# Optimization experiments

Measured on AMD Instinct MI355X. Metric: run time of the kernel, lower is better.

Reference implementation:

```python
import jax, jax.numpy as jnp
import numpy as np

EMB, KDIM, B, S = 1024, 64, 8, 2048

def setup_inputs() -> dict:
    key = jax.random.key(0)
    kx, kq, kk, kv1, kv2 = jax.random.split(key, 5)
    def xavier(k, shape):
        fan_in, fan_out = shape
        lim = (6.0 / (fan_in + fan_out)) ** 0.5
        return jax.random.uniform(k, shape, jnp.float32, -lim, lim)
    return {
        "x": jax.random.normal(kx, (B, S, EMB), jnp.float32),
        "w_q": xavier(kq, (EMB, KDIM)),
        "w_k": xavier(kk, (EMB, KDIM)),
        "w_v1": xavier(kv1, (EMB, KDIM)),
        "w_v2": xavier(kv2, (KDIM, EMB)),
    }

def reference(x, w_q, w_k, w_v1, w_v2) -> jnp.ndarray:
    # x: [B, S, E]
    seq = x.shape[1]
    queries = jnp.einsum("bse,ek->bsk", x, w_q)
    keys = jnp.einsum("bse,ek->bsk", x, w_k)
    scale = w_q.shape[1] ** -0.5
    scores = jnp.einsum("bqk,bsk->bqs", queries, keys) * scale  # [B, S, S]
    causal = jnp.tril(jnp.ones((seq, seq), dtype=bool))  # True = keep
    scores = jnp.where(causal[None, :, :], scores, -jnp.inf)
    attn = jax.nn.softmax(scores, axis=-1)
    values = jnp.einsum("bsk,ke->bse", jnp.einsum("bse,ek->bsk", x, w_v1), w_v2)
    return jnp.einsum("bqs,bse->bqe", attn, values)
```

## Files before the change

### kernel.cpp

```cpp
#include <hip/hip_runtime.h>

typedef _Float16 f16_t;
typedef __attribute__((ext_vector_type(8))) _Float16 f16x8;
typedef __attribute__((ext_vector_type(4))) _Float16 f16x4;
typedef __attribute__((ext_vector_type(4))) float f32x4;

#define MFMA16(a, b, c) __builtin_amdgcn_mfma_f32_16x16x32_f16((a), (b), (c), 0, 0, 0)


extern "C" __global__ __launch_bounds__(256) void prep_k(
    const float* __restrict__ wq, const float* __restrict__ wk,
    const float* __restrict__ wv1, const float* __restrict__ wv2,
    f16_t* __restrict__ WT, f16_t* __restrict__ WV2T) {
  int idx = blockIdx.x * 256 + threadIdx.x;
  if (idx < 196608) {
    int j = idx >> 16;
    int r = idx & 65535;
    int n = r >> 10;
    int e = r & 1023;
    const float* w = (j == 0) ? wq : ((j == 1) ? wk : wv1);
    float v = w[e * 64 + n];
    if (j == 0) v *= 0.125f;
    WT[idx] = (f16_t)v;
  } else if (idx < 262144) {
    int r = idx - 196608;
    int e = r >> 6, k = r & 63;
    WV2T[r] = (f16_t)wv2[k * 1024 + e];
  }
}

extern "C" __global__ __launch_bounds__(256) void proj_k(
    const float* __restrict__ x, const f16_t* __restrict__ WT,
    f16_t* __restrict__ Qg, f16_t* __restrict__ Kg, f16_t* __restrict__ Vtg) {
  __shared__ __align__(16) f16_t xs[64][72];
  __shared__ __align__(16) f16_t wsh[192][72];
  const int t = threadIdx.x;
  const int wave = t >> 6, lane = t & 63;
  const int quad = lane >> 4, ln = lane & 15;
  const int r0 = blockIdx.x * 64;

  f32x4 acc[4][3];
#pragma unroll
  for (int mt = 0; mt < 4; ++mt)
#pragma unroll
    for (int nn = 0; nn < 3; ++nn) acc[mt][nn] = (f32x4){0.f, 0.f, 0.f, 0.f};

  float4 xreg[4];
  f16x8 wreg[6];
#pragma unroll
  for (int i = 0; i < 4; ++i) {
    int flat = t + i * 256;
    int row = flat >> 4, c4 = (flat & 15) * 4;
    xreg[i] = *(const float4*)&x[(size_t)(r0 + row) * 1024 + c4];
  }
#pragma unroll
  for (int i = 0; i < 6; ++i) {
    int flat = t + i * 256;
    int row = flat >> 3, c8 = (flat & 7) * 8;
    wreg[i] = *(const f16x8*)&WT[row * 1024 + c8];
  }

  for (int ec = 0; ec < 16; ++ec) {
    __syncthreads();
#pragma unroll
    for (int i = 0; i < 4; ++i) {
      int flat = t + i * 256;
      int row = flat >> 4, c4 = (flat & 15) * 4;
      f16x4 h;
      h[0] = (f16_t)xreg[i].x; h[1] = (f16_t)xreg[i].y;
      h[2] = (f16_t)xreg[i].z; h[3] = (f16_t)xreg[i].w;
      *(f16x4*)&xs[row][c4] = h;
    }
#pragma unroll
    for (int i = 0; i < 6; ++i) {
      int flat = t + i * 256;
      int row = flat >> 3, c8 = (flat & 7) * 8;
      *(f16x8*)&wsh[row][c8] = wreg[i];
    }
    __syncthreads();
    if (ec < 15) {
      int e0 = (ec + 1) * 64;
#pragma unroll
      for (int i = 0; i < 4; ++i) {
        int flat = t + i * 256;
        int row = flat >> 4, c4 = (flat & 15) * 4;
        xreg[i] = *(const float4*)&x[(size_t)(r0 + row) * 1024 + e0 + c4];
      }
#pragma unroll
      for (int i = 0; i < 6; ++i) {
        int flat = t + i * 256;
        int row = flat >> 3, c8 = (flat & 7) * 8;
        wreg[i] = *(const f16x8*)&WT[row * 1024 + e0 + c8];
      }
    }
    f16x8 a0[4], a1[4];
#pragma unroll
    for (int mt = 0; mt < 4; ++mt) {
      a0[mt] = *(const f16x8*)&xs[mt * 16 + ln][quad * 8];
      a1[mt] = *(const f16x8*)&xs[mt * 16 + ln][32 + quad * 8];
    }
#pragma unroll
    for (int nn = 0; nn < 3; ++nn) {
      int nb = (wave * 3 + nn) * 16;
      f16x8 b0 = *(const f16x8*)&wsh[nb + ln][quad * 8];
      f16x8 b1 = *(const f16x8*)&wsh[nb + ln][32 + quad * 8];
#pragma unroll
      for (int mt = 0; mt < 4; ++mt) {
        acc[mt][nn] = MFMA16(a0[mt], b0, acc[mt][nn]);
        acc[mt][nn] = MFMA16(a1[mt], b1, acc[mt][nn]);
      }
    }
  }

  __syncthreads();
  f16_t* vt = &xs[0][0];
#pragma unroll
  for (int nn = 0; nn < 3; ++nn) {
    int col = (wave * 3 + nn) * 16 + ln;
    int j = col >> 6, cc = col & 63;
#pragma unroll
    for (int mt = 0; mt < 4; ++mt)
#pragma unroll
      for (int r = 0; r < 4; ++r) {
        int row = mt * 16 + quad * 4 + r;
        f16_t hv = (f16_t)acc[mt][nn][r];
        if (j == 0)      Qg[(size_t)(r0 + row) * 64 + cc] = hv;
        else if (j == 1) Kg[(size_t)(r0 + row) * 64 + cc] = hv;
        else             vt[cc * 72 + row] = hv;
      }
  }
  __syncthreads();
  {
    int bb = r0 >> 11, sblk = r0 & 2047;
#pragma unroll
    for (int i = 0; i < 2; ++i) {
      int flat = t + i * 256;
      int vrow = flat >> 3, c8 = (flat & 7) * 8;
      *(f16x8*)&Vtg[((size_t)bb * 64 + vrow) * 2048 + sblk + c8] =
          *(const f16x8*)&vt[vrow * 72 + c8];
    }
  }
}

extern "C" __global__ __launch_bounds__(256) void flash_k(
    const f16_t* __restrict__ Qg, const f16_t* __restrict__ Kg,
    const f16_t* __restrict__ Vtg, f16_t* __restrict__ O1) {
  __shared__ __align__(16) f16_t Ks[64][72];
  __shared__ __align__(16) f16_t Vs[64][72];
  __shared__ __align__(16) f16_t Ps[4][16][72];
  const int t = threadIdx.x;
  const int wave = t >> 6, lane = t & 63;
  const int quad = lane >> 4, ln = lane & 15;
  const int b = blockIdx.x >> 5, qt = blockIdx.x & 31;
  const int q0 = qt * 64;
  const size_t rbase = (size_t)b * 2048;

  f16x8 qa0, qa1;
  {
    size_t row = rbase + q0 + wave * 16 + ln;
    qa0 = *(const f16x8*)&Qg[row * 64 + quad * 8];
    qa1 = *(const f16x8*)&Qg[row * 64 + 32 + quad * 8];
  }
  float m[4], lsum[4];
  f32x4 oacc[4];
#pragma unroll
  for (int r = 0; r < 4; ++r) { m[r] = -__builtin_inff(); lsum[r] = 0.f; }
#pragma unroll
  for (int nt = 0; nt < 4; ++nt) oacc[nt] = (f32x4){0.f, 0.f, 0.f, 0.f};

  f16x8 kreg[2], vreg[2];
#pragma unroll
  for (int i = 0; i < 2; ++i) {
    int flat = t + i * 256;
    int row = flat >> 3, c8 = (flat & 7) * 8;
    kreg[i] = *(const f16x8*)&Kg[(rbase + row) * 64 + c8];
    vreg[i] = *(const f16x8*)&Vtg[((size_t)b * 64 + row) * 2048 + c8];
  }

  for (int st = 0; st <= qt; ++st) {
    __syncthreads();
#pragma unroll
    for (int i = 0; i < 2; ++i) {
      int flat = t + i * 256;
      int row = flat >> 3, c8 = (flat & 7) * 8;
      *(f16x8*)&Ks[row][c8] = kreg[i];
      *(f16x8*)&Vs[row][c8] = vreg[i];
    }
    __syncthreads();
    if (st < qt) {
      int s0n = (st + 1) * 64;
#pragma unroll
      for (int i = 0; i < 2; ++i) {
        int flat = t + i * 256;
        int row = flat >> 3, c8 = (flat & 7) * 8;
        kreg[i] = *(const f16x8*)&Kg[(rbase + s0n + row) * 64 + c8];
        vreg[i] = *(const f16x8*)&Vtg[((size_t)b * 64 + row) * 2048 + s0n + c8];
      }
    }
    f32x4 sc[4];
#pragma unroll
    for (int nt = 0; nt < 4; ++nt) {
      f16x8 b0 = *(const f16x8*)&Ks[nt * 16 + ln][quad * 8];
      f16x8 b1 = *(const f16x8*)&Ks[nt * 16 + ln][32 + quad * 8];
      f32x4 c = (f32x4){0.f, 0.f, 0.f, 0.f};
      c = MFMA16(qa0, b0, c);
      c = MFMA16(qa1, b1, c);
      sc[nt] = c;
    }
    if (st == qt) {
#pragma unroll
      for (int nt = 0; nt < 4; ++nt)
#pragma unroll
        for (int r = 0; r < 4; ++r)
          if (nt * 16 + ln > wave * 16 + quad * 4 + r) sc[nt][r] = -__builtin_inff();
    }
    float alpha[4], mn[4];
#pragma unroll
    for (int r = 0; r < 4; ++r) {
      float mx = fmaxf(fmaxf(sc[0][r], sc[1][r]), fmaxf(sc[2][r], sc[3][r]));
      mx = fmaxf(mx, __shfl_xor(mx, 1, 64));
      mx = fmaxf(mx, __shfl_xor(mx, 2, 64));
      mx = fmaxf(mx, __shfl_xor(mx, 4, 64));
      mx = fmaxf(mx, __shfl_xor(mx, 8, 64));
      mn[r] = fmaxf(m[r], mx);
      alpha[r] = __expf(m[r] - mn[r]);
      m[r] = mn[r];
    }
    float p[4][4];
#pragma unroll
    for (int nt = 0; nt < 4; ++nt)
#pragma unroll
      for (int r = 0; r < 4; ++r) p[nt][r] = __expf(sc[nt][r] - mn[r]);
#pragma unroll
    for (int r = 0; r < 4; ++r) {
      float s = (p[0][r] + p[1][r]) + (p[2][r] + p[3][r]);
      s += __shfl_xor(s, 1, 64);
      s += __shfl_xor(s, 2, 64);
      s += __shfl_xor(s, 4, 64);
      s += __shfl_xor(s, 8, 64);
      lsum[r] = lsum[r] * alpha[r] + s;
    }
#pragma unroll
    for (int nt = 0; nt < 4; ++nt)
#pragma unroll
      for (int r = 0; r < 4; ++r) oacc[nt][r] *= alpha[r];
#pragma unroll
    for (int nt = 0; nt < 4; ++nt)
#pragma unroll
      for (int r = 0; r < 4; ++r)
        Ps[wave][quad * 4 + r][nt * 16 + ln] = (f16_t)p[nt][r];
    f16x8 pa0 = *(const f16x8*)&Ps[wave][ln][quad * 8];
    f16x8 pa1 = *(const f16x8*)&Ps[wave][ln][32 + quad * 8];
#pragma unroll
    for (int nt = 0; nt < 4; ++nt) {
      f16x8 v0 = *(const f16x8*)&Vs[nt * 16 + ln][quad * 8];
      f16x8 v1 = *(const f16x8*)&Vs[nt * 16 + ln][32 + quad * 8];
      oacc[nt] = MFMA16(pa0, v0, oacc[nt]);
      oacc[nt] = MFMA16(pa1, v1, oacc[nt]);
    }
  }
  float inv[4];
#pragma unroll
  for (int r = 0; r < 4; ++r) inv[r] = 1.0f / lsum[r];
#pragma unroll
  for (int nt = 0; nt < 4; ++nt)
#pragma unroll
    for (int r = 0; r < 4; ++r) {
      size_t row = rbase + q0 + wave * 16 + quad * 4 + r;
      O1[row * 64 + nt * 16 + ln] = (f16_t)(oacc[nt][r] * inv[r]);
    }
}

extern "C" __global__ __launch_bounds__(256) void fproj_k(
    const f16_t* __restrict__ O1, const f16_t* __restrict__ WV2T,
    float* __restrict__ out) {
  const int t = threadIdx.x;
  const int wave = t >> 6, lane = t & 63;
  const int quad = lane >> 4, ln = lane & 15;
  const int r0 = blockIdx.x * 64;
  f16x8 a0[4], a1[4];
#pragma unroll
  for (int mt = 0; mt < 4; ++mt) {
    size_t row = (size_t)(r0 + mt * 16 + ln);
    a0[mt] = *(const f16x8*)&O1[row * 64 + quad * 8];
    a1[mt] = *(const f16x8*)&O1[row * 64 + 32 + quad * 8];
  }
#pragma unroll 4
  for (int nt = 0; nt < 16; ++nt) {
    int eb = wave * 256 + nt * 16;
    f16x8 b0 = *(const f16x8*)&WV2T[(eb + ln) * 64 + quad * 8];
    f16x8 b1 = *(const f16x8*)&WV2T[(eb + ln) * 64 + 32 + quad * 8];
#pragma unroll
    for (int mt = 0; mt < 4; ++mt) {
      f32x4 c = (f32x4){0.f, 0.f, 0.f, 0.f};
      c = MFMA16(a0[mt], b0, c);
      c = MFMA16(a1[mt], b1, c);
#pragma unroll
      for (int r = 0; r < 4; ++r)
        out[(size_t)(r0 + mt * 16 + quad * 4 + r) * 1024 + eb + ln] = c[r];
    }
  }
}

extern "C" void kernel_launch(void* const* d_in, const int* in_sizes, int n_in,
                              void* d_out, int out_size, void* d_ws, size_t ws_size,
                              hipStream_t stream) {
  const float* x   = (const float*)d_in[0];
  const float* wq  = (const float*)d_in[1];
  const float* wk  = (const float*)d_in[2];
  const float* wv1 = (const float*)d_in[3];
  const float* wv2 = (const float*)d_in[4];
  float* out = (float*)d_out;

  f16_t* WT   = (f16_t*)d_ws;
  f16_t* WV2T = WT + 196608;
  f16_t* Qg   = WV2T + 65536;
  f16_t* Kg   = Qg + 1048576;
  f16_t* Vtg  = Kg + 1048576;
  f16_t* O1   = Vtg + 1048576;

  prep_k <<<1024, 256, 0, stream>>>(wq, wk, wv1, wv2, WT, WV2T);
  proj_k <<<256, 256, 0, stream>>>(x, WT, Qg, Kg, Vtg);
  flash_k<<<256, 256, 0, stream>>>(Qg, Kg, Vtg, O1);
  fproj_k<<<256, 256, 0, stream>>>(O1, WV2T, out);
}
```

Before: 180.3 us.

## Split attention KV range across blocks with merge pass; halve projection tiles

The flash kernel now splits each query tile's causal key range into chunks of 8 key tiles, handled by separate blocks. Each block writes unnormalized partial outputs plus its row max and sum, and a new merge kernel combines them with log-sum-exp weighting. Projection and final-projection kernels use 32-row tiles, which doubles their grid size. The aim is to fix the low occupancy and causal load imbalance of 256 blocks on a large GPU, at the cost of partial-buffer traffic, an extra launch, and fp16 rounding of the unnormalized partials.

```diff
diff --git a/kernel.cpp b/kernel.cpp
--- a/kernel.cpp
+++ b/kernel.cpp
@@ -32,23 +32,23 @@
 extern "C" __global__ __launch_bounds__(256) void proj_k(
     const float* __restrict__ x, const f16_t* __restrict__ WT,
     f16_t* __restrict__ Qg, f16_t* __restrict__ Kg, f16_t* __restrict__ Vtg) {
-  __shared__ __align__(16) f16_t xs[64][72];
+  __shared__ __align__(16) f16_t xs[32][72];
   __shared__ __align__(16) f16_t wsh[192][72];
   const int t = threadIdx.x;
   const int wave = t >> 6, lane = t & 63;
   const int quad = lane >> 4, ln = lane & 15;
-  const int r0 = blockIdx.x * 64;
-
-  f32x4 acc[4][3];
-#pragma unroll
-  for (int mt = 0; mt < 4; ++mt)
+  const int r0 = blockIdx.x * 32;
+
+  f32x4 acc[2][3];
+#pragma unroll
+  for (int mt = 0; mt < 2; ++mt)
 #pragma unroll
     for (int nn = 0; nn < 3; ++nn) acc[mt][nn] = (f32x4){0.f, 0.f, 0.f, 0.f};
 
-  float4 xreg[4];
+  float4 xreg[2];
   f16x8 wreg[6];
 #pragma unroll
-  for (int i = 0; i < 4; ++i) {
+  for (int i = 0; i < 2; ++i) {
     int flat = t + i * 256;
     int row = flat >> 4, c4 = (flat & 15) * 4;
     xreg[i] = *(const float4*)&x[(size_t)(r0 + row) * 1024 + c4];
@@ -63,7 +63,7 @@
   for (int ec = 0; ec < 16; ++ec) {
     __syncthreads();
 #pragma unroll
-    for (int i = 0; i < 4; ++i) {
+    for (int i = 0; i < 2; ++i) {
       int flat = t + i * 256;
       int row = flat >> 4, c4 = (flat & 15) * 4;
       f16x4 h;
@@ -81,7 +81,7 @@
     if (ec < 15) {
       int e0 = (ec + 1) * 64;
 #pragma unroll
-      for (int i = 0; i < 4; ++i) {
+      for (int i = 0; i < 2; ++i) {
         int flat = t + i * 256;
         int row = flat >> 4, c4 = (flat & 15) * 4;
         xreg[i] = *(const float4*)&x[(size_t)(r0 + row) * 1024 + e0 + c4];
@@ -93,9 +93,9 @@
         wreg[i] = *(const f16x8*)&WT[row * 1024 + e0 + c8];
       }
     }
-    f16x8 a0[4], a1[4];
-#pragma unroll
-    for (int mt = 0; mt < 4; ++mt) {
+    f16x8 a0[2], a1[2];
+#pragma unroll
+    for (int mt = 0; mt < 2; ++mt) {
       a0[mt] = *(const f16x8*)&xs[mt * 16 + ln][quad * 8];
       a1[mt] = *(const f16x8*)&xs[mt * 16 + ln][32 + quad * 8];
     }
@@ -105,7 +105,7 @@
       f16x8 b0 = *(const f16x8*)&wsh[nb + ln][quad * 8];
       f16x8 b1 = *(const f16x8*)&wsh[nb + ln][32 + quad * 8];
 #pragma unroll
-      for (int mt = 0; mt < 4; ++mt) {
+      for (int mt = 0; mt < 2; ++mt) {
         acc[mt][nn] = MFMA16(a0[mt], b0, acc[mt][nn]);
         acc[mt][nn] = MFMA16(a1[mt], b1, acc[mt][nn]);
       }
@@ -113,45 +113,47 @@
   }
 
   __syncthreads();
-  f16_t* vt = &xs[0][0];
+  f16_t* vt = &wsh[0][0];
 #pragma unroll
   for (int nn = 0; nn < 3; ++nn) {
     int col = (wave * 3 + nn) * 16 + ln;
     int j = col >> 6, cc = col & 63;
 #pragma unroll
-    for (int mt = 0; mt < 4; ++mt)
+    for (int mt = 0; mt < 2; ++mt)
 #pragma unroll
       for (int r = 0; r < 4; ++r) {
         int row = mt * 16 + quad * 4 + r;
         f16_t hv = (f16_t)acc[mt][nn][r];
         if (j == 0)      Qg[(size_t)(r0 + row) * 64 + cc] = hv;
         else if (j == 1) Kg[(size_t)(r0 + row) * 64 + cc] = hv;
-        else             vt[cc * 72 + row] = hv;
+        else             vt[cc * 40 + row] = hv;
       }
   }
   __syncthreads();
   {
     int bb = r0 >> 11, sblk = r0 & 2047;
-#pragma unroll
-    for (int i = 0; i < 2; ++i) {
-      int flat = t + i * 256;
-      int vrow = flat >> 3, c8 = (flat & 7) * 8;
-      *(f16x8*)&Vtg[((size_t)bb * 64 + vrow) * 2048 + sblk + c8] =
-          *(const f16x8*)&vt[vrow * 72 + c8];
-    }
+    int vrow = t >> 2, c8 = (t & 3) * 8;
+    *(f16x8*)&Vtg[((size_t)bb * 64 + vrow) * 2048 + sblk + c8] =
+        *(const f16x8*)&vt[vrow * 40 + c8];
   }
 }
 
 extern "C" __global__ __launch_bounds__(256) void flash_k(
     const f16_t* __restrict__ Qg, const f16_t* __restrict__ Kg,
-    const f16_t* __restrict__ Vtg, f16_t* __restrict__ O1) {
+    const f16_t* __restrict__ Vtg, f16_t* __restrict__ Opart,
+    float* __restrict__ Mpart, float* __restrict__ Lpart) {
+  const int bi = blockIdx.x;
+  const int b = bi >> 7, qt = (bi >> 2) & 31, c = bi & 3;
+  const int st0 = c * 8;
+  if (st0 > qt) return;
+  const int stEnd = (qt < st0 + 7) ? qt : (st0 + 7);
+
   __shared__ __align__(16) f16_t Ks[64][72];
   __shared__ __align__(16) f16_t Vs[64][72];
   __shared__ __align__(16) f16_t Ps[4][16][72];
   const int t = threadIdx.x;
   const int wave = t >> 6, lane = t & 63;
   const int quad = lane >> 4, ln = lane & 15;
-  const int b = blockIdx.x >> 5, qt = blockIdx.x & 31;
   const int q0 = qt * 64;
   const size_t rbase = (size_t)b * 2048;
 
@@ -173,11 +175,11 @@
   for (int i = 0; i < 2; ++i) {
     int flat = t + i * 256;
     int row = flat >> 3, c8 = (flat & 7) * 8;
-    kreg[i] = *(const f16x8*)&Kg[(rbase + row) * 64 + c8];
-    vreg[i] = *(const f16x8*)&Vtg[((size_t)b * 64 + row) * 2048 + c8];
-  }
-
-  for (int st = 0; st <= qt; ++st) {
+    kreg[i] = *(const f16x8*)&Kg[(rbase + st0 * 64 + row) * 64 + c8];
+    vreg[i] = *(const f16x8*)&Vtg[((size_t)b * 64 + row) * 2048 + st0 * 64 + c8];
+  }
+
+  for (int st = st0; st <= stEnd; ++st) {
     __syncthreads();
 #pragma unroll
     for (int i = 0; i < 2; ++i) {
@@ -187,7 +189,7 @@
       *(f16x8*)&Vs[row][c8] = vreg[i];
     }
     __syncthreads();
-    if (st < qt) {
+    if (st < stEnd) {
       int s0n = (st + 1) * 64;
 #pragma unroll
       for (int i = 0; i < 2; ++i) {
@@ -202,10 +204,10 @@
     for (int nt = 0; nt < 4; ++nt) {
       f16x8 b0 = *(const f16x8*)&Ks[nt * 16 + ln][quad * 8];
       f16x8 b1 = *(const f16x8*)&Ks[nt * 16 + ln][32 + quad * 8];
-      f32x4 c = (f32x4){0.f, 0.f, 0.f, 0.f};
-      c = MFMA16(qa0, b0, c);
-      c = MFMA16(qa1, b1, c);
-      sc[nt] = c;
+      f32x4 cc = (f32x4){0.f, 0.f, 0.f, 0.f};
+      cc = MFMA16(qa0, b0, cc);
+      cc = MFMA16(qa1, b1, cc);
+      sc[nt] = cc;
     }
     if (st == qt) {
 #pragma unroll
@@ -259,16 +261,63 @@
       oacc[nt] = MFMA16(pa1, v1, oacc[nt]);
     }
   }
-  float inv[4];
-#pragma unroll
-  for (int r = 0; r < 4; ++r) inv[r] = 1.0f / lsum[r];
+  const size_t pid = (size_t)bi;
 #pragma unroll
   for (int nt = 0; nt < 4; ++nt)
 #pragma unroll
     for (int r = 0; r < 4; ++r) {
-      size_t row = rbase + q0 + wave * 16 + quad * 4 + r;
-      O1[row * 64 + nt * 16 + ln] = (f16_t)(oacc[nt][r] * inv[r]);
-    }
+      int qrow = wave * 16 + quad * 4 + r;
+      Opart[pid * 4096 + (size_t)qrow * 64 + nt * 16 + ln] = (f16_t)oacc[nt][r];
+    }
+  if (ln == 0) {
+#pragma unroll
+    for (int r = 0; r < 4; ++r) {
+      int qrow = wave * 16 + quad * 4 + r;
+      Mpart[pid * 64 + qrow] = m[r];
+      Lpart[pid * 64 + qrow] = lsum[r];
+    }
+  }
+}
+
+extern "C" __global__ __launch_bounds__(256) void merge_k(
+    const f16_t* __restrict__ Opart, const float* __restrict__ Mpart,
+    const float* __restrict__ Lpart, f16_t* __restrict__ O1) {
+  const int t = threadIdx.x;
+  const int b = blockIdx.x >> 5, qt = blockIdx.x & 31;
+  const int q = t >> 2, vq = (t & 3) * 16;
+  const int pbase = b * 128 + qt * 4;
+  const int nc = (qt >> 3) + 1;
+  float m[4], l[4], M = -1e30f;
+  for (int c = 0; c < nc; ++c) {
+    m[c] = Mpart[(size_t)(pbase + c) * 64 + q];
+    l[c] = Lpart[(size_t)(pbase + c) * 64 + q];
+    M = fmaxf(M, m[c]);
+  }
+  float denom = 0.f;
+  float acc[16];
+#pragma unroll
+  for (int k = 0; k < 16; ++k) acc[k] = 0.f;
+  for (int c = 0; c < nc; ++c) {
+    float w = __expf(m[c] - M);
+    denom += w * l[c];
+    const f16_t* src = &Opart[(size_t)(pbase + c) * 4096 + q * 64 + vq];
+    f16x8 o0 = *(const f16x8*)src;
+    f16x8 o1 = *(const f16x8*)(src + 8);
+#pragma unroll
+    for (int k = 0; k < 8; ++k) acc[k] += w * (float)o0[k];
+#pragma unroll
+    for (int k = 0; k < 8; ++k) acc[k + 8] += w * (float)o1[k];
+  }
+  float inv = 1.0f / denom;
+  f16x8 r0, r1;
+#pragma unroll
+  for (int k = 0; k < 8; ++k) {
+    r0[k] = (f16_t)(acc[k] * inv);
+    r1[k] = (f16_t)(acc[k + 8] * inv);
+  }
+  size_t row = (size_t)b * 2048 + qt * 64 + q;
+  *(f16x8*)&O1[row * 64 + vq] = r0;
+  *(f16x8*)&O1[row * 64 + vq + 8] = r1;
 }
 
 extern "C" __global__ __launch_bounds__(256) void fproj_k(
@@ -277,10 +326,10 @@
   const int t = threadIdx.x;
   const int wave = t >> 6, lane = t & 63;
   const int quad = lane >> 4, ln = lane & 15;
-  const int r0 = blockIdx.x * 64;
-  f16x8 a0[4], a1[4];
-#pragma unroll
-  for (int mt = 0; mt < 4; ++mt) {
+  const int r0 = blockIdx.x * 32;
+  f16x8 a0[2], a1[2];
+#pragma unroll
+  for (int mt = 0; mt < 2; ++mt) {
     size_t row = (size_t)(r0 + mt * 16 + ln);
     a0[mt] = *(const f16x8*)&O1[row * 64 + quad * 8];
     a1[mt] = *(const f16x8*)&O1[row * 64 + 32 + quad * 8];
@@ -291,13 +340,13 @@
     f16x8 b0 = *(const f16x8*)&WV2T[(eb + ln) * 64 + quad * 8];
     f16x8 b1 = *(const f16x8*)&WV2T[(eb + ln) * 64 + 32 + quad * 8];
 #pragma unroll
-    for (int mt = 0; mt < 4; ++mt) {
-      f32x4 c = (f32x4){0.f, 0.f, 0.f, 0.f};
-      c = MFMA16(a0[mt], b0, c);
-      c = MFMA16(a1[mt], b1, c);
+    for (int mt = 0; mt < 2; ++mt) {
+      f32x4 cc = (f32x4){0.f, 0.f, 0.f, 0.f};
+      cc = MFMA16(a0[mt], b0, cc);
+      cc = MFMA16(a1[mt], b1, cc);
 #pragma unroll
       for (int r = 0; r < 4; ++r)
-        out[(size_t)(r0 + mt * 16 + quad * 4 + r) * 1024 + eb + ln] = c[r];
+        out[(size_t)(r0 + mt * 16 + quad * 4 + r) * 1024 + eb + ln] = cc[r];
     }
   }
 }
@@ -312,15 +361,19 @@
   const float* wv2 = (const float*)d_in[4];
   float* out = (float*)d_out;
 
-  f16_t* WT   = (f16_t*)d_ws;
-  f16_t* WV2T = WT + 196608;
-  f16_t* Qg   = WV2T + 65536;
-  f16_t* Kg   = Qg + 1048576;
-  f16_t* Vtg  = Kg + 1048576;
-  f16_t* O1   = Vtg + 1048576;
+  f16_t* WT    = (f16_t*)d_ws;
+  f16_t* WV2T  = WT + 196608;
+  f16_t* Qg    = WV2T + 65536;
+  f16_t* Kg    = Qg + 1048576;
+  f16_t* Vtg   = Kg + 1048576;
+  f16_t* O1    = Vtg + 1048576;
+  f16_t* Opart = O1 + 1048576;
+  float* Mpart = (float*)(Opart + 4194304);
+  float* Lpart = Mpart + 65536;
 
   prep_k <<<1024, 256, 0, stream>>>(wq, wk, wv1, wv2, WT, WV2T);
-  proj_k <<<256, 256, 0, stream>>>(x, WT, Qg, Kg, Vtg);
-  flash_k<<<256, 256, 0, stream>>>(Qg, Kg, Vtg, O1);
-  fproj_k<<<256, 256, 0, stream>>>(O1, WV2T, out);
-}
+  proj_k <<<512, 256, 0, stream>>>(x, WT, Qg, Kg, Vtg);
+  flash_k<<<1024, 256, 0, stream>>>(Qg, Kg, Vtg, Opart, Mpart, Lpart);
+  merge_k<<<256, 256, 0, stream>>>(Opart, Mpart, Lpart, O1);
+  fproj_k<<<512, 256, 0, stream>>>(O1, WV2T, out);
+}
```

After: 178.4 us. Within noise of the previous version (-1.1%).
